# Optimization experiments

Hardware: AMD Instinct MI355X
Metric: run time of the kernel (lower is better)

## Reference

```python
import jax, jax.numpy as jnp
import numpy as np

B, S, E, D, H, L = 128, 50, 512, 1024, 16, 4
V, NU, NF, NR = 100000, 50000, 10000, 5
DK = D // H
FF = 4 * D


def _pe(S, D):
    # FranchisePositionalEncoding: two interleaved sin/cos halves (chrono + release*1.5)
    half = D // 2
    pos = jnp.arange(S, dtype=jnp.float32)[:, None]
    div = jnp.exp(jnp.arange(0, half, 2, dtype=jnp.float32) * (-np.log(10000.0) / half))
    def il(a):
        return jnp.stack([jnp.sin(a), jnp.cos(a)], axis=-1).reshape(S, half)
    return jnp.concatenate([il(pos * div), il(pos * div * 1.5)], axis=-1)  # [S, D]


def _ln(x, g, b):
    m = x.mean(-1, keepdims=True)
    v = ((x - m) ** 2).mean(-1, keepdims=True)
    return (x - m) * jax.lax.rsqrt(v + 1e-5) * g + b


def _gelu(x):
    return jax.nn.gelu(x, approximate=False)


def setup_inputs() -> dict:
    key = jax.random.key(0)
    ks = iter(jax.random.split(key, 64))
    def p(shape, s=0.02):
        return jax.random.normal(next(ks), shape, jnp.float32) * s
    inp = {
        'movie_table': p((V, E)), 'fran_table': p((NF, E)), 'entry_table': p((NR, E)),
        'proj_w': p((3 * E, D)), 'proj_b': jnp.zeros((D,), jnp.float32),
        'wq': p((L, D, D)), 'bq': jnp.zeros((L, D), jnp.float32),
        'wk': p((L, D, D)), 'bk': jnp.zeros((L, D), jnp.float32),
        'wv': p((L, D, D)), 'bv': jnp.zeros((L, D), jnp.float32),
        'wo': p((L, D, D)), 'bo': jnp.zeros((L, D), jnp.float32),
        'rel_table': p((L, NR, DK)),
        'aln_g': jnp.ones((L, D), jnp.float32), 'aln_b': jnp.zeros((L, D), jnp.float32),
        'f_w1': p((L, D, FF)), 'f_b1': jnp.zeros((L, FF), jnp.float32),
        'f_w2': p((L, FF, D)), 'f_b2': jnp.zeros((L, D), jnp.float32),
        'ln_g': jnp.ones((L, D), jnp.float32), 'ln_b': jnp.zeros((L, D), jnp.float32),
        'user_table': p((NU, D)),
        'mq_w': p((D, D)), 'mq_b': jnp.zeros((D,), jnp.float32),
        'mk_w': p((D, D)), 'mk_b': jnp.zeros((D,), jnp.float32),
        'mv_w': p((D, D)), 'mv_b': jnp.zeros((D,), jnp.float32),
        'mo_w': p((D, D)), 'mo_b': jnp.zeros((D,), jnp.float32),
        'c_w1': p((2 * D, D)), 'c_b1': jnp.zeros((D,), jnp.float32),
        'c_w2': p((D, 1)), 'c_b2': jnp.zeros((1,), jnp.float32),
        'n_w1': p((2 * D, D)), 'n_b1': jnp.zeros((D,), jnp.float32),
        'n_w2': p((D, V)), 'n_b2': jnp.zeros((V,), jnp.float32),
        'r_w1': p((3 * D, D)), 'r_b1': jnp.zeros((D,), jnp.float32),
        'r_w2': p((D, 1)), 'r_b2': jnp.zeros((1,), jnp.float32),
        'o_w1': p((D, D // 2)), 'o_b1': jnp.zeros((D // 2,), jnp.float32),
        'o_w2': p((D // 2, 2)), 'o_b2': jnp.zeros((2,), jnp.float32),
        'user_ids': jax.random.randint(next(ks), (B,), 0, NU),
        'movie_ids': jax.random.randint(next(ks), (B, S), 0, V),
        'franchise_ids': jax.random.randint(next(ks), (B, S), 0, NF),
        'entry_types': jax.random.randint(next(ks), (B, S), 0, NR),
        'relation_matrix': jax.random.randint(next(ks), (S, S), 0, NR),
    }
    return inp


def reference(movie_table, fran_table, entry_table, proj_w, proj_b,
              wq, bq, wk, bk, wv, bv, wo, bo, rel_table, aln_g, aln_b,
              f_w1, f_b1, f_w2, f_b2, ln_g, ln_b, user_table,
              mq_w, mq_b, mk_w, mk_b, mv_w, mv_b, mo_w, mo_b,
              c_w1, c_b1, c_w2, c_b2, n_w1, n_b1, n_w2, n_b2,
              r_w1, r_b1, r_w2, r_b2, o_w1, o_b1, o_w2, o_b2,
              user_ids, movie_ids, franchise_ids, entry_types, relation_matrix):
    b, s = movie_ids.shape
    d = proj_w.shape[1]
    nl, _, dk = rel_table.shape
    h = d // dk
    scale = 1.0 / np.sqrt(dk).astype(np.float32)

    # encoder input: concat(movie, franchise, entry) embeddings -> proj -> +PE
    x = jnp.concatenate([movie_table[movie_ids], fran_table[franchise_ids],
                         entry_table[entry_types]], axis=-1) @ proj_w + proj_b
    x = x + _pe(s, d)

    for l in range(nl):
        res = x
        q = (x @ wq[l] + bq[l]).reshape(b, s, h, dk).transpose(0, 2, 1, 3)  # [b,h,s,dk]
        k = (x @ wk[l] + bk[l]).reshape(b, s, h, dk).transpose(0, 2, 1, 3)
        v = (x @ wv[l] + bv[l]).reshape(b, s, h, dk).transpose(0, 2, 1, 3)
        scores = jnp.einsum('bhid,bhjd->bhij', q, k) * scale
        rel = rel_table[l][relation_matrix]  # [s,s,dk]
        scores = scores + 0.5 * jnp.einsum('bhid,ijd->bhij', q, rel)
        attn = jax.nn.softmax(scores, axis=-1)
        ctx = jnp.einsum('bhij,bhjd->bhid', attn, v).transpose(0, 2, 1, 3).reshape(b, s, d)
        x = _ln(ctx @ wo[l] + bo[l] + res, aln_g[l], aln_b[l])
        ff = _gelu(x @ f_w1[l] + f_b1[l]) @ f_w2[l] + f_b2[l]
        x = _ln(x + ff, ln_g[l], ln_b[l])

    # user preference cross-attention (nn.MultiheadAttention, q_len=1)
    user_emb = user_table[user_ids]  # [b,d]
    qh = (user_emb @ mq_w + mq_b).reshape(b, h, dk)
    kh = (x @ mk_w + mk_b).reshape(b, s, h, dk)
    vh = (x @ mv_w + mv_b).reshape(b, s, h, dk)
    a = jax.nn.softmax(jnp.einsum('bhd,bshd->bhs', qh, kh) * scale, axis=-1)
    user_pref = jnp.einsum('bhs,bshd->bhd', a, vh).reshape(b, d) @ mo_w + mo_b

    seq_repr = x.mean(axis=1)  # mask is None path
    ci = jnp.concatenate([user_pref, seq_repr], axis=-1)
    completion = jax.nn.sigmoid(_gelu(ci @ c_w1 + c_b1) @ c_w2 + c_b2)
    next_logits = _gelu(ci @ n_w1 + n_b1) @ n_w2 + n_b2
    ri = jnp.concatenate([user_emb, user_pref, seq_repr], axis=-1)
    rating = _gelu(ri @ r_w1 + r_b1) @ r_w2 + r_b2
    order = jax.nn.softmax(_gelu(user_pref @ o_w1 + o_b1) @ o_w2 + o_b2, axis=-1)
    return (x, completion, next_logits, rating, order, user_pref)
```

## Files before the change

kernel.cpp:

```cpp
#include <hip/hip_runtime.h>
#include <hip/hip_bf16.h>
#include <math.h>

#define B_   128
#define S_   50
#define BS_  (B_*S_)
#define E_   512
#define D_   1024
#define H_   16
#define DK_  64
#define L_   4
#define FF_  4096
#define V_   100000

typedef short bf8_t __attribute__((ext_vector_type(8)));
typedef float f32x4 __attribute__((ext_vector_type(4)));
typedef unsigned short u16;

__device__ __forceinline__ float gelu_exact(float x) {
    return 0.5f * x * (1.0f + erff(x * 0.70710678118654752440f));
}
__device__ __forceinline__ u16 f2bf(float f) {
    unsigned int u = __float_as_uint(f);
    return (u16)((u + 0x7FFFu + ((u >> 16) & 1u)) >> 16);
// ... 85 lines not shown
    const float* __restrict__ cb1, const float* __restrict__ nb1,
    const float* __restrict__ mkb, const float* __restrict__ mvb,
    float* __restrict__ bqkv, float* __restrict__ bcn, float* __restrict__ bkv,
    float* __restrict__ pet)
{
    int bi = blockIdx.x, tid = threadIdx.x;
    if (bi < 4) {
        for (int c = tid; c < 3072; c += 256) {
            float v = (c < 1024) ? bq[bi * 1024 + c]
                    : (c < 2048) ? bk[bi * 1024 + c - 1024]
                                 : bv[bi * 1024 + c - 2048];
            bqkv[bi * 3072 + c] = v;
        }
    } else if (bi == 4) {
        for (int c = tid; c < 2048; c += 256)
            bcn[c] = (c < 1024) ? cb1[c] : nb1[c - 1024];
    } else if (bi == 5) {
        for (int c = tid; c < 2048; c += 256)
            bkv[c] = (c < 1024) ? mkb[c] : mvb[c - 1024];
    } else {
        int s = bi - 6;
        const float cc = -logf(10000.0f) / 512.0f;
        for (int d = tid; d < D_; d += 256) {
            int second = d >= 512;
            int c2 = second ? d - 512 : d;
            int i = c2 >> 1;
            float div = expf(cc * (float)(2 * i));
            float aa = (float)s * div * (second ? 1.5f : 1.0f);
            pet[s * D_ + d] = (c2 & 1) ? cosf(aa) : sinf(aa);
        }
    }
}

template<int BM>
__global__ __launch_bounds__(256) void gemm_bf16_t(
    const u16* __restrict__ A, int lda, const u16* __restrict__ Wt,
    const float* __restrict__ bias, float* __restrict__ Cf,
    u16* __restrict__ Cb, int ldcb, u16* __restrict__ Cb2, int ldcb2,
    int N, int K, int act, const float* __restrict__ pe)
{
    constexpr int MR   = BM / 32;
    constexpr int AL   = BM / 64;
    constexpr int ABUF = BM * 32;
    __shared__ u16 As[2 * ABUF];
    __shared__ u16 Bs[2 * 4096];
    const int tid  = threadIdx.x;
    const int lane = tid & 63;
    const int wid  = tid >> 6;
    const int wr   = wid >> 1, wc = wid & 1;

    const int gx  = gridDim.x;
    const int nwg = gx * gridDim.y;
    int orig = blockIdx.y * gx + blockIdx.x;
    int qq = nwg >> 3, rr2 = nwg & 7, xcd = orig & 7, idx = orig >> 3;
    int wgid = (xcd < rr2) ? (xcd * (qq + 1) + idx)
                           : (rr2 * (qq + 1) + (xcd - rr2) * qq + idx);
    const int rowBase = (wgid / gx) * BM;
    const int colBase = (wgid % gx) * 128;

    const int fr = lane & 15;
    const int hi = lane >> 4;

    const int sRowL  = lane >> 2;
    const int sChunk = lane & 3;
    const int aRow0 = wid * (BM / 4) + sRowL;
    const int aKey  = (aRow0 >> 1) & 3;
    const u16* aS0 = A + (size_t)(rowBase + aRow0) * lda + ((sChunk ^ aKey) << 3);
    const u16* aS1 = aS0 + (size_t)16 * lda;
    const int ldsA0 = (wid * (BM / 4)) * 32;
    const int ldsA1 = ldsA0 + 512;
    const int bRow0 = wid * 32 + sRowL;
    const int bKey  = (bRow0 >> 1) & 3;
    const u16* bS0 = Wt + (size_t)(colBase + bRow0) * K + ((sChunk ^ bKey) << 3);
    const u16* bS1 = bS0 + (size_t)16 * K;
    const int ldsB0 = (wid * 32) * 32;
    const int ldsB1 = ldsB0 + 512;

    const int swz = ((hi ^ ((fr >> 1) & 3)) << 3);
    const int aRd = (wr * (BM / 2) + fr) * 32 + swz;
    const int bRd = (wc * 64 + fr) * 32 + swz;

    f32x4 acc[MR][4] = {};
    const int nk = K >> 5;

    auto STAGE = [&](int kb, int buf) {
        u16* dA = As + buf * ABUF;
        u16* dB = Bs + buf * 4096;
        gload16(aS0 + kb, dA + ldsA0);
        if constexpr (AL == 2) gload16(aS1 + kb, dA + ldsA1);
        gload16(bS0 + kb, dB + ldsB0);
        gload16(bS1 + kb, dB + ldsB1);
// ... 20 lines not shown
            bf[n] = *reinterpret_cast<const bf8_t*>(&bB[bRd + n * 512]);
        #pragma unroll
        for (int m = 0; m < MR; ++m)
            #pragma unroll
            for (int n = 0; n < 4; ++n)
                acc[m][n] = __builtin_amdgcn_mfma_f32_16x16x32_bf16(af[m], bf[n], acc[m][n], 0, 0, 0);
        if (t == nk - 1) break;
        __builtin_amdgcn_sched_barrier(0);
        asm volatile("s_waitcnt lgkmcnt(0)\n\ts_barrier" ::: "memory");
        __builtin_amdgcn_sched_barrier(0);
        if (t + 2 < nk) {
            STAGE((t + 2) << 5, cur);
            __builtin_amdgcn_sched_barrier(0);
            if constexpr (BM == 128) asm volatile("s_waitcnt vmcnt(4)\n\ts_barrier" ::: "memory");
            else                     asm volatile("s_waitcnt vmcnt(3)\n\ts_barrier" ::: "memory");
        } else {
            asm volatile("s_waitcnt vmcnt(0)\n\ts_barrier" ::: "memory");
        }
        __builtin_amdgcn_sched_barrier(0);
    }

    const int orow = hi << 2;
    #pragma unroll
    for (int m = 0; m < MR; ++m) {
        int r0 = rowBase + wr * (BM / 2) + m * 16 + orow;
        #pragma unroll
        for (int n = 0; n < 4; ++n) {
            int c = colBase + wc * 64 + n * 16 + fr;
            float bv = bias ? bias[c] : 0.0f;
            #pragma unroll
            for (int r = 0; r < 4; ++r) {
                float v = acc[m][n][r] + bv;
                if (act == 1) v = gelu_exact(v);
                if (pe) v += pe[(size_t)((r0 + r) % S_) * N + c];
                if (Cf)  Cf [(size_t)(r0 + r) * N + c] = v;
                if (Cb)  Cb [(size_t)(r0 + r) * ldcb  + c] = f2bf(v);
                if (Cb2) Cb2[(size_t)(r0 + r) * ldcb2 + c] = f2bf(v);
            }
        }
    }
}

__global__ __launch_bounds__(256) void gemm_logits(
    const float* __restrict__ A, int lda, const float* __restrict__ W,
    const float* __restrict__ bias, float* __restrict__ C, int N, int K)
{
    __shared__ u16 As[2][128][40];
    __shared__ u16 Bs[2][128][40];
    const int tid  = threadIdx.x;
    const int lane = tid & 63;
    const int wid  = tid >> 6;
    const int wr   = wid >> 1, wc = wid & 1;
    const int colBase = blockIdx.x * 128;

    const int a_r = tid >> 1;
    const int a_h = (tid & 1) << 4;
    const int b_c = tid & 127;
    const int b_h = (tid >> 7) << 4;

    const int fr = lane & 15;
    const int fk = (lane >> 4) << 3;

    f32x4 acc[4][4] = {};
    const int nvalid = N - colBase;
    const bool valid = b_c < nvalid;
    const int nk = K >> 5;

    float4 aR[4];
    float  bR[16];

    auto LD = [&](int kb) {
        const float* Ap = A + (size_t)a_r * lda + kb + a_h;
        #pragma unroll
        for (int q = 0; q < 4; ++q)
            aR[q] = *reinterpret_cast<const float4*>(Ap + q * 4);
        const float* Wp = W + (size_t)(kb + b_h) * N + colBase + b_c;
        #pragma unroll
        for (int kk = 0; kk < 16; ++kk)
            bR[kk] = valid ? Wp[(size_t)kk * N] : 0.0f;
    };
    auto ST = [&](int buf) {
        #pragma unroll
        for (int q = 0; q < 4; ++q) {
            ushort4 bb;
            bb.x = f2bf(aR[q].x); bb.y = f2bf(aR[q].y);
            bb.z = f2bf(aR[q].z); bb.w = f2bf(aR[q].w);
            *reinterpret_cast<ushort4*>(&As[buf][a_r][a_h + q * 4]) = bb;
        }
        u16 tmp[16];
        #pragma unroll
        for (int kk = 0; kk < 16; ++kk) tmp[kk] = f2bf(bR[kk]);
        *reinterpret_cast<bf8_t*>(&Bs[buf][b_c][b_h])     = *reinterpret_cast<const bf8_t*>(tmp);
        *reinterpret_cast<bf8_t*>(&Bs[buf][b_c][b_h + 8]) = *reinterpret_cast<const bf8_t*>(tmp + 8);
    };

    LD(0); ST(0);
    __syncthreads();

    for (int t = 0; t < nk; ++t) {
        if (t + 1 < nk) LD((t + 1) << 5);
        const int cur = t & 1;
        bf8_t af[4], bfv[4];
        #pragma unroll
        for (int m = 0; m < 4; ++m)
            af[m] = *reinterpret_cast<const bf8_t*>(&As[cur][wr * 64 + m * 16 + fr][fk]);
        #pragma unroll
        for (int n = 0; n < 4; ++n)
            bfv[n] = *reinterpret_cast<const bf8_t*>(&Bs[cur][wc * 64 + n * 16 + fr][fk]);
        #pragma unroll
        for (int m = 0; m < 4; ++m)
            #pragma unroll
            for (int n = 0; n < 4; ++n)
                acc[m][n] = __builtin_amdgcn_mfma_f32_16x16x32_bf16(af[m], bfv[n], acc[m][n], 0, 0, 0);
        if (t + 1 < nk) ST(cur ^ 1);
        __syncthreads();
    }

    const int orow = (lane >> 4) << 2;
    #pragma unroll
    for (int m = 0; m < 4; ++m) {
        int r0 = wr * 64 + m * 16 + orow;
        #pragma unroll
        for (int n = 0; n < 4; ++n) {
            int c = colBase + wc * 64 + n * 16 + fr;
            if (c < N) {
                float bv = bias ? bias[c] : 0.0f;
                #pragma unroll
                for (int r = 0; r < 4; ++r)
                    C[(size_t)(r0 + r) * N + c] = acc[m][n][r] + bv;
            }
        }
    }
}

__global__ __launch_bounds__(256) void attn_kernel(
    const u16* __restrict__ qkv, const float* __restrict__ rt, const int* __restrict__ rm,
    u16* __restrict__ ctxb)
{
    int bh = blockIdx.x;
    int b = bh >> 4, h = bh & 15;
    __shared__ float qs[S_][DK_ + 1], ks[S_][DK_ + 1], vs[S_][DK_ + 1];
    __shared__ float rts[5][DK_];
    __shared__ float Rs[S_][8];
    int tid = threadIdx.x;
    int wave = tid >> 6, lane = tid & 63;

    for (int idx = tid; idx < S_ * DK_; idx += 256) {
        int s = idx >> 6, d = idx & 63;
        size_t g = ((size_t)(b * S_ + s)) * (3 * D_) + h * DK_ + d;
        qs[s][d] = bf2f(qkv[g]);
        ks[s][d] = bf2f(qkv[g + D_]);
        vs[s][d] = bf2f(qkv[g + 2 * D_]);
    }
    for (int i = tid; i < 5 * DK_; i += 256)
        rts[i >> 6][i & 63] = rt[i];
    __syncthreads();

    for (int t = tid; t < S_ * 5; t += 256) {
        int i = t / 5, r = t - 5 * i;
        float a = 0.0f;
        #pragma unroll 8
        for (int d = 0; d < DK_; ++d) a += qs[i][d] * rts[r][d];
        Rs[i][r] = a;
    }
    __syncthreads();

    const float scale = 0.125f;
    for (int i = wave; i < S_; i += 4) {
        float sc = -INFINITY;
        if (lane < S_) {
            float acc = 0.0f;
            #pragma unroll 8
            for (int d = 0; d < DK_; ++d) acc += qs[i][d] * ks[lane][d];
            sc = acc * scale + 0.5f * Rs[i][rm[i * S_ + lane]];
        }
        float m = sc;
        #pragma unroll
        for (int off = 32; off; off >>= 1) m = fmaxf(m, __shfl_xor(m, off));
        float e = (lane < S_) ? expf(sc - m) : 0.0f;
        float sum = e;
        #pragma unroll
        for (int off = 32; off; off >>= 1) sum += __shfl_xor(sum, off);
        float aval = e / sum;

        float acc = 0.0f;
        for (int j = 0; j < S_; ++j) {
            float aj = __shfl(aval, j);
            acc += aj * vs[j][lane];
        }
        ctxb[((size_t)(b * S_ + i)) * D_ + h * DK_ + lane] = f2bf(acc);
    }
}

__global__ __launch_bounds__(256) void add_ln(
    const u16* __restrict__ a, const u16* __restrict__ res,
    const float* __restrict__ g, const float* __restrict__ be,
    u16* __restrict__ outb, float* __restrict__ outf)
{
    int row = blockIdx.x, tid = threadIdx.x;
    int c0 = tid << 2;
    ushort4 va = *reinterpret_cast<const ushort4*>(a   + (size_t)row * D_ + c0);
    ushort4 vr = *reinterpret_cast<const ushort4*>(res + (size_t)row * D_ + c0);
    float vals[4] = { bf2f(va.x) + bf2f(vr.x), bf2f(va.y) + bf2f(vr.y),
                      bf2f(va.z) + bf2f(vr.z), bf2f(va.w) + bf2f(vr.w) };
    float s = vals[0] + vals[1] + vals[2] + vals[3];
    __shared__ float red[8];
    #pragma unroll
    for (int off = 32; off; off >>= 1) s += __shfl_xor(s, off);
    int wave = tid >> 6, lane = tid & 63;
    if (lane == 0) red[wave] = s;
    __syncthreads();
    float mean = (red[0] + red[1] + red[2] + red[3]) * (1.0f / D_);
    float vv = 0.0f;
    #pragma unroll
    for (int t = 0; t < 4; ++t) {
        float d = vals[t] - mean;
        vv += d * d;
    }
    #pragma unroll
    for (int off = 32; off; off >>= 1) vv += __shfl_xor(vv, off);
    if (lane == 0) red[4 + wave] = vv;
    __syncthreads();
    float var = (red[4] + red[5] + red[6] + red[7]) * (1.0f / D_);
    float rstd = rsqrtf(var + 1e-5f);
    float4 gv  = *reinterpret_cast<const float4*>(g  + c0);
    float4 bev = *reinterpret_cast<const float4*>(be + c0);
    float o0 = (vals[0] - mean) * rstd * gv.x + bev.x;
    float o1 = (vals[1] - mean) * rstd * gv.y + bev.y;
    float o2 = (vals[2] - mean) * rstd * gv.z + bev.z;
    float o3 = (vals[3] - mean) * rstd * gv.w + bev.w;
    ushort4 ob;
    ob.x = f2bf(o0); ob.y = f2bf(o1); ob.z = f2bf(o2); ob.w = f2bf(o3);
    *reinterpret_cast<ushort4*>(outb + (size_t)row * D_ + c0) = ob;
    if (outf) {
        float4 of = { o0, o1, o2, o3 };
        *reinterpret_cast<float4*>(outf + (size_t)row * D_ + c0) = of;
    }
}

__global__ __launch_bounds__(256) void gather_user(
    const float* __restrict__ ut, const int* __restrict__ ids,
    u16* __restrict__ o1, int ld1, u16* __restrict__ o2, int ld2)
{
    int b = blockIdx.x;
    int uid = ids[b];
    for (int d = threadIdx.x; d < D_; d += 256) {
        u16 v = f2bf(ut[(size_t)uid * D_ + d]);
        o1[(size_t)b * ld1 + d] = v;
        o2[(size_t)b * ld2 + d] = v;
    }
}

__global__ __launch_bounds__(64) void cross_attn(
    const u16* __restrict__ qh, const u16* __restrict__ kv, u16* __restrict__ up)
{
    int bh = blockIdx.x;
    int b = bh >> 4, h = bh & 15;
    int lane = threadIdx.x;
    __shared__ float qv[DK_];
    qv[lane] = bf2f(qh[(size_t)b * D_ + h * DK_ + lane]);
    __syncthreads();
    float sc = -INFINITY;
    if (lane < S_) {
        float acc = 0.0f;
        const u16* krow = kv + ((size_t)(b * S_ + lane)) * 2048 + h * DK_;
        #pragma unroll 8
        for (int d = 0; d < DK_; ++d) acc += qv[d] * bf2f(krow[d]);
        sc = acc * 0.125f;
    }
// ... 115 lines not shown
    const float* r_b1        = (const float*)d_in[40];
    const float* r_w2        = (const float*)d_in[41];
    const float* r_b2        = (const float*)d_in[42];
    const float* o_w1        = (const float*)d_in[43];
    const float* o_b1        = (const float*)d_in[44];
    const float* o_w2        = (const float*)d_in[45];
    const float* o_b2        = (const float*)d_in[46];
    const int* user_ids      = (const int*)d_in[47];
    const int* movie_ids     = (const int*)d_in[48];
    const int* franchise_ids = (const int*)d_in[49];
    const int* entry_types   = (const int*)d_in[50];
    const int* relation_mat  = (const int*)d_in[51];

    u16* up16 = (u16*)d_ws;
    u16* proj_wt = up16;
    u16* wqkv_t  = proj_wt + (size_t)1024 * 1536;
    u16* wo_t    = wqkv_t  + (size_t)4 * 3072 * 1024;
    u16* fw1_buf = wo_t    + (size_t)4 * 1024 * 1024;
    u16* fw2_buf = fw1_buf + (size_t)4096 * 1024;
    u16* mq_t    = fw2_buf + (size_t)1024 * 4096;
    u16* mk_t    = mq_t    + (size_t)1024 * 1024;
    u16* mv_t    = mk_t    + (size_t)1024 * 1024;
    u16* mo_t    = mv_t    + (size_t)1024 * 1024;
    u16* cn_w1t  = mo_t    + (size_t)1024 * 1024;
    u16* r_w1t   = cn_w1t  + (size_t)2048 * 2048;
    u16* o_w1t   = r_w1t   + (size_t)1024 * 3072;
    u16* ffb     = o_w1t   + (size_t)512 * 1024;
    u16* xinb    = ffb;
    u16* xb      = ffb     + (size_t)BS_ * FF_;
    u16* xb2     = xb      + (size_t)BS_ * D_;
    u16* qkvb    = xb2     + (size_t)BS_ * D_;
    u16* kvb     = qkvb    + (size_t)BS_ * 3 * D_;
    u16* ctxb    = kvb;
    u16* ob      = kvb     + (size_t)BS_ * D_;
    u16* ueb     = kvb     + (size_t)BS_ * 2 * D_;
    u16* upb_pre = ueb     + (size_t)B_ * D_;
    u16* cib     = upb_pre + (size_t)B_ * D_;
    u16* rib     = cib     + (size_t)B_ * 2 * D_;
    float* fp    = (float*)(rib + (size_t)B_ * 3 * D_);
    float* bqkv  = fp;
    float* bcn   = bqkv + 4 * 3072;
    float* bkv   = bcn  + 2048;
    float* pet   = bkv  + 2048;
    float* h1cn  = pet  + 50 * 1024;
    float* h1r   = h1cn + (size_t)B_ * 2048;
    float* ho    = h1r  + (size_t)B_ * D_;

    float* xout    = (float*)d_out;
    float* comp    = xout + (size_t)BS_ * D_;
    float* logits  = comp + B_;
    float* rating  = logits + (size_t)B_ * V_;
    float* order   = rating + B_;
    float* upref   = order + 2 * B_;

    dim3 blk(256);

    wtrans<<<dim3(32, 48, 1), blk, 0, stream>>>(proj_w, proj_wt, 1536, 1024, 0, 0, 0);
    wtrans_qkv<<<dim3(32, 32, 12), blk, 0, stream>>>(wq, wk, wv, wqkv_t);
    WT8 w8;
    w8.s[0] = wo;                 w8.d[0] = wo_t;
    w8.s[1] = wo + 1048576;       w8.d[1] = wo_t + 1048576;
    w8.s[2] = wo + 2097152;       w8.d[2] = wo_t + 2097152;
    w8.s[3] = wo + 3145728;       w8.d[3] = wo_t + 3145728;
    w8.s[4] = mq_w;               w8.d[4] = mq_t;
    w8.s[5] = mk_w;               w8.d[5] = mk_t;
    w8.s[6] = mv_w;               w8.d[6] = mv_t;
    w8.s[7] = mo_w;               w8.d[7] = mo_t;
    wtrans8<<<dim3(32, 32, 8), blk, 0, stream>>>(w8);
    wtrans<<<dim3(32, 64, 1), blk, 0, stream>>>(c_w1, cn_w1t, 2048, 1024, 0, 0, 0);
    wtrans<<<dim3(32, 64, 1), blk, 0, stream>>>(n_w1, cn_w1t, 2048, 1024, 0, 0, 1024);
    wtrans<<<dim3(32, 96, 1), blk, 0, stream>>>(r_w1, r_w1t, 3072, 1024, 0, 0, 0);
    wtrans<<<dim3(16, 32, 1), blk, 0, stream>>>(o_w1, o_w1t, 1024, 512, 0, 0, 0);
    setup_misc<<<dim3(56), blk, 0, stream>>>(bq, bk, bv, c_b1, n_b1, mk_b, mv_b,
                                             bqkv, bcn, bkv, pet);

    embed_concat<<<BS_, blk, 0, stream>>>(movie_table, fran_table, entry_table,
                                          movie_ids, franchise_ids, entry_types, xinb);
    gemm_bf16_t<64><<<dim3(8, 100), blk, 0, stream>>>(xinb, 1536, proj_wt, proj_b,
                                                      nullptr, xb, 1024, nullptr, 0,
                                                      D_, 1536, 0, pet);

    for (int l = 0; l < L_; ++l) {
        gemm_bf16_t<128><<<dim3(24, 50), blk, 0, stream>>>(xb, 1024,
                wqkv_t + (size_t)l * 3145728, bqkv + l * 3072,
                nullptr, qkvb, 3072, nullptr, 0, 3 * D_, D_, 0, nullptr);
        attn_kernel<<<B_ * H_, blk, 0, stream>>>(qkvb, rel_table + (size_t)l * 5 * DK_,
                                                 relation_mat, ctxb);
        gemm_bf16_t<64><<<dim3(8, 100), blk, 0, stream>>>(ctxb, 1024,
                wo_t + (size_t)l * 1048576, bo + l * D_,
                nullptr, ob, 1024, nullptr, 0, D_, D_, 0, nullptr);
        add_ln<<<BS_, blk, 0, stream>>>(ob, xb, aln_g + l * D_, aln_b + l * D_, xb2, nullptr);
        wtrans_ff<<<dim3(128, 32, 2), blk, 0, stream>>>(f_w1 + (size_t)l * D_ * FF_,
                                                        f_w2 + (size_t)l * FF_ * D_,
                                                        fw1_buf, fw2_buf);
        gemm_bf16_t<128><<<dim3(32, 50), blk, 0, stream>>>(xb2, 1024, fw1_buf, f_b1 + l * FF_,
                nullptr, ffb, 4096, nullptr, 0, FF_, D_, 1, nullptr);
        gemm_bf16_t<64><<<dim3(8, 100), blk, 0, stream>>>(ffb, 4096, fw2_buf, f_b2 + l * D_,
                nullptr, ob, 1024, nullptr, 0, D_, FF_, 0, nullptr);
        add_ln<<<BS_, blk, 0, stream>>>(ob, xb2, ln_g + l * D_, ln_b + l * D_, xb,
                                        (l == L_ - 1) ? xout : nullptr);
    }

    gather_user<<<B_, blk, 0, stream>>>(user_table, user_ids, ueb, 1024, rib, 3072);
    gemm_bf16_t<64><<<dim3(8, 2), blk, 0, stream>>>(ueb, 1024, mq_t, mq_b,
            nullptr, qkvb, 1024, nullptr, 0, D_, D_, 0, nullptr);
    gemm_bf16_t<64><<<dim3(16, 100), blk, 0, stream>>>(xb, 1024, mk_t, bkv,
            nullptr, kvb, 2048, nullptr, 0, 2 * D_, D_, 0, nullptr);
    cross_attn<<<B_ * H_, dim3(64), 0, stream>>>(qkvb, kvb, upb_pre);
    gemm_bf16_t<64><<<dim3(8, 2), blk, 0, stream>>>(upb_pre, 1024, mo_t, mo_b,
            upref, cib, 2048, rib + 1024, 3072, D_, D_, 0, nullptr);

    seq_mean<<<B_, blk, 0, stream>>>(xout, cib + 1024, 2048, rib + 2048, 3072);

    gemm_bf16_t<64><<<dim3(16, 2), blk, 0, stream>>>(cib, 2048, cn_w1t, bcn,
            h1cn, nullptr, 0, nullptr, 0, 2048, 2048, 1, nullptr);
    gemm_bf16_t<64><<<dim3(8, 2), blk, 0, stream>>>(rib, 3072, r_w1t, r_b1,
            h1r, nullptr, 0, nullptr, 0, D_, 3072, 1, nullptr);
    gemm_bf16_t<64><<<dim3(4, 2), blk, 0, stream>>>(cib, 2048, o_w1t, o_b1,
            ho, nullptr, 0, nullptr, 0, 512, D_, 1, nullptr);
    gemm_logits<<<dim3(782, 1), blk, 0, stream>>>(h1cn + 1024, 2048, n_w2, n_b2,
                                                  logits, V_, D_);
    heads_final<<<B_, blk, 0, stream>>>(h1cn, h1r, ho, c_w2, c_b2, r_w2, r_b2,
                                        o_w2, o_b2, comp, rating, order);
}
```

Measured before the change: 2.283 ms.

## Split-K 128x128 GEMM for N=1024 projections with fused bias/residual LayerNorm combine

Replaces the 64-row-tile GEMMs with N=1024 outputs (input projection, Wo, FF2) by a 128x128 split-K kernel. The kernel splits K in two across blockIdx.z, writes fp32 partials, and reorders workgroups to be XCD-aware. The partials are summed with bias (plus positional encoding or residual add and LayerNorm) in new combine kernels. The cross-attention KV GEMM also moves to 128-row tiles. This aims to raise per-block data reuse while keeping enough blocks in flight, at the cost of extra fp32 partial traffic that reuses scratch buffers.

```diff
diff --git a/kernel.cpp b/kernel.cpp
--- a/kernel.cpp
+++ b/kernel.cpp
@@ -261,168 +261,148 @@
     }
 }
 
-__global__ __launch_bounds__(256) void gemm_logits(
-    const float* __restrict__ A, int lda, const float* __restrict__ W,
-    const float* __restrict__ bias, float* __restrict__ C, int N, int K)
-{
-    __shared__ u16 As[2][128][40];
-    __shared__ u16 Bs[2][128][40];
+__global__ __launch_bounds__(256) void gemm_sk(
+    const u16* __restrict__ A, int lda, const u16* __restrict__ Wt, int ldb,
+    float* __restrict__ P0, float* __restrict__ P1,
+    int N, int Kh)
+{
+    __shared__ u16 As[2 * 4096];
+    __shared__ u16 Bs[2 * 4096];
     const int tid  = threadIdx.x;
     const int lane = tid & 63;
     const int wid  = tid >> 6;
     const int wr   = wid >> 1, wc = wid & 1;
-    const int colBase = blockIdx.x * 128;
-
-    const int a_r = tid >> 1;
-    const int a_h = (tid & 1) << 4;
-    const int b_c = tid & 127;
-    const int b_h = (tid >> 7) << 4;
+
+    const int gx  = gridDim.x;
+    const int nwg = gx * gridDim.y;
+    int orig = blockIdx.y * gx + blockIdx.x;
+    int qq = nwg >> 3, rr2 = nwg & 7, xcd = orig & 7, idx = orig >> 3;
+    int wgid = (xcd < rr2) ? (xcd * (qq + 1) + idx)
+                           : (rr2 * (qq + 1) + (xcd - rr2) * qq + idx);
+    const int rowBase = (wgid / gx) * 128;
+    const int colBase = (wgid % gx) * 128;
+    const int k0 = blockIdx.z * Kh;
+    float* P = blockIdx.z ? P1 : P0;
 
     const int fr = lane & 15;
-    const int fk = (lane >> 4) << 3;
+    const int hi = lane >> 4;
+
+    const int sRowL  = lane >> 2;
+    const int sChunk = lane & 3;
+    const int gRow0  = (wid << 5) + sRowL;
+    const int skey   = (gRow0 >> 1) & 3;
+    const int gC     = (sChunk ^ skey) << 3;
+    const u16* aS0 = A  + (size_t)(rowBase + gRow0) * lda + k0 + gC;
+    const u16* aS1 = aS0 + (size_t)16 * lda;
+    const u16* bS0 = Wt + (size_t)(colBase + gRow0) * ldb + k0 + gC;
+    const u16* bS1 = bS0 + (size_t)16 * ldb;
+    const int ldsW0 = (wid << 5) << 5;
+    const int ldsW1 = ldsW0 + (16 << 5);
+
+    const int swz = ((hi ^ ((fr >> 1) & 3)) << 3);
+    const int aRd = (wr * 64 + fr) * 32 + swz;
+    const int bRd = (wc * 64 + fr) * 32 + swz;
 
     f32x4 acc[4][4] = {};
-    const int nvalid = N - colBase;
-    const bool valid = b_c < nvalid;
-    const int nk = K >> 5;
-
-    float4 aR[4];
-    float  bR[16];
-
-    auto LD = [&](int kb) {
-        const float* Ap = A + (size_t)a_r * lda + kb + a_h;
-        #pragma unroll
-        for (int q = 0; q < 4; ++q)
-            aR[q] = *reinterpret_cast<const float4*>(Ap + q * 4);
-        const float* Wp = W + (size_t)(kb + b_h) * N + colBase + b_c;
-        #pragma unroll
-        for (int kk = 0; kk < 16; ++kk)
-            bR[kk] = valid ? Wp[(size_t)kk * N] : 0.0f;
+    const int nk = Kh >> 5;
+
+    auto STAGE = [&](int kb, int buf) {
+        u16* dA = As + buf * 4096;
+        u16* dB = Bs + buf * 4096;
+        gload16(aS0 + kb, dA + ldsW0);
+        gload16(aS1 + kb, dA + ldsW1);
+        gload16(bS0 + kb, dB + ldsW0);
+        gload16(bS1 + kb, dB + ldsW1);
     };
-    auto ST = [&](int buf) {
-        #pragma unroll
-        for (int q = 0; q < 4; ++q) {
-            ushort4 bb;
-            bb.x = f2bf(aR[q].x); bb.y = f2bf(aR[q].y);
-            bb.z = f2bf(aR[q].z); bb.w = f2bf(aR[q].w);
-            *reinterpret_cast<ushort4*>(&As[buf][a_r][a_h + q * 4]) = bb;
-        }
-        u16 tmp[16];
-        #pragma unroll
-        for (int kk = 0; kk < 16; ++kk) tmp[kk] = f2bf(bR[kk]);
-        *reinterpret_cast<bf8_t*>(&Bs[buf][b_c][b_h])     = *reinterpret_cast<const bf8_t*>(tmp);
-        *reinterpret_cast<bf8_t*>(&Bs[buf][b_c][b_h + 8]) = *reinterpret_cast<const bf8_t*>(tmp + 8);
-    };
-
-    LD(0); ST(0);
-    __syncthreads();
+
+    STAGE(0, 0);
+    __builtin_amdgcn_sched_barrier(0);
+    STAGE(32, 1);
+    __builtin_amdgcn_sched_barrier(0);
+    asm volatile("s_waitcnt vmcnt(4)\n\ts_barrier" ::: "memory");
+    __builtin_amdgcn_sched_barrier(0);
 
     for (int t = 0; t < nk; ++t) {
-        if (t + 1 < nk) LD((t + 1) << 5);
         const int cur = t & 1;
-        bf8_t af[4], bfv[4];
+        const u16* bA = As + cur * 4096;
+        const u16* bB = Bs + cur * 4096;
+        bf8_t af[4], bf[4];
         #pragma unroll
         for (int m = 0; m < 4; ++m)
-            af[m] = *reinterpret_cast<const bf8_t*>(&As[cur][wr * 64 + m * 16 + fr][fk]);
+            af[m] = *reinterpret_cast<const bf8_t*>(&bA[aRd + m * 512]);
         #pragma unroll
         for (int n = 0; n < 4; ++n)
-            bfv[n] = *reinterpret_cast<const bf8_t*>(&Bs[cur][wc * 64 + n * 16 + fr][fk]);
+            bf[n] = *reinterpret_cast<const bf8_t*>(&bB[bRd + n * 512]);
         #pragma unroll
         for (int m = 0; m < 4; ++m)
             #pragma unroll
             for (int n = 0; n < 4; ++n)
-                acc[m][n] = __builtin_amdgcn_mfma_f32_16x16x32_bf16(af[m], bfv[n], acc[m][n], 0, 0, 0);
-        if (t + 1 < nk) ST(cur ^ 1);
-        __syncthreads();
-    }
-
-    const int orow = (lane >> 4) << 2;
+                acc[m][n] = __builtin_amdgcn_mfma_f32_16x16x32_bf16(af[m], bf[n], acc[m][n], 0, 0, 0);
+        if (t == nk - 1) break;
+        __builtin_amdgcn_sched_barrier(0);
+        asm volatile("s_waitcnt lgkmcnt(0)\n\ts_barrier" ::: "memory");
+        __builtin_amdgcn_sched_barrier(0);
+        if (t + 2 < nk) {
+            STAGE((t + 2) << 5, cur);
+            __builtin_amdgcn_sched_barrier(0);
+            asm volatile("s_waitcnt vmcnt(4)\n\ts_barrier" ::: "memory");
+        } else {
+            asm volatile("s_waitcnt vmcnt(0)\n\ts_barrier" ::: "memory");
+        }
+        __builtin_amdgcn_sched_barrier(0);
+    }
+
+    const int orow = hi << 2;
     #pragma unroll
     for (int m = 0; m < 4; ++m) {
-        int r0 = wr * 64 + m * 16 + orow;
+        int r0 = rowBase + wr * 64 + m * 16 + orow;
         #pragma unroll
         for (int n = 0; n < 4; ++n) {
             int c = colBase + wc * 64 + n * 16 + fr;
-            if (c < N) {
-                float bv = bias ? bias[c] : 0.0f;
-                #pragma unroll
-                for (int r = 0; r < 4; ++r)
-                    C[(size_t)(r0 + r) * N + c] = acc[m][n][r] + bv;
-            }
-        }
-    }
-}
-
-__global__ __launch_bounds__(256) void attn_kernel(
-    const u16* __restrict__ qkv, const float* __restrict__ rt, const int* __restrict__ rm,
-    u16* __restrict__ ctxb)
-{
-    int bh = blockIdx.x;
-    int b = bh >> 4, h = bh & 15;
-    __shared__ float qs[S_][DK_ + 1], ks[S_][DK_ + 1], vs[S_][DK_ + 1];
-    __shared__ float rts[5][DK_];
-    __shared__ float Rs[S_][8];
-    int tid = threadIdx.x;
-    int wave = tid >> 6, lane = tid & 63;
-
-    for (int idx = tid; idx < S_ * DK_; idx += 256) {
-        int s = idx >> 6, d = idx & 63;
-        size_t g = ((size_t)(b * S_ + s)) * (3 * D_) + h * DK_ + d;
-        qs[s][d] = bf2f(qkv[g]);
-        ks[s][d] = bf2f(qkv[g + D_]);
-        vs[s][d] = bf2f(qkv[g + 2 * D_]);
-    }
-    for (int i = tid; i < 5 * DK_; i += 256)
-        rts[i >> 6][i & 63] = rt[i];
-    __syncthreads();
-
-    for (int t = tid; t < S_ * 5; t += 256) {
-        int i = t / 5, r = t - 5 * i;
-        float a = 0.0f;
-        #pragma unroll 8
-        for (int d = 0; d < DK_; ++d) a += qs[i][d] * rts[r][d];
-        Rs[i][r] = a;
-    }
-    __syncthreads();
-
-    const float scale = 0.125f;
-    for (int i = wave; i < S_; i += 4) {
-        float sc = -INFINITY;
-        if (lane < S_) {
-            float acc = 0.0f;
-            #pragma unroll 8
-            for (int d = 0; d < DK_; ++d) acc += qs[i][d] * ks[lane][d];
-            sc = acc * scale + 0.5f * Rs[i][rm[i * S_ + lane]];
-        }
-        float m = sc;
-        #pragma unroll
-        for (int off = 32; off; off >>= 1) m = fmaxf(m, __shfl_xor(m, off));
-        float e = (lane < S_) ? expf(sc - m) : 0.0f;
-        float sum = e;
-        #pragma unroll
-        for (int off = 32; off; off >>= 1) sum += __shfl_xor(sum, off);
-        float aval = e / sum;
-
-        float acc = 0.0f;
-        for (int j = 0; j < S_; ++j) {
-            float aj = __shfl(aval, j);
-            acc += aj * vs[j][lane];
-        }
-        ctxb[((size_t)(b * S_ + i)) * D_ + h * DK_ + lane] = f2bf(acc);
-    }
-}
-
-__global__ __launch_bounds__(256) void add_ln(
-    const u16* __restrict__ a, const u16* __restrict__ res,
+            #pragma unroll
+            for (int r = 0; r < 4; ++r)
+                P[(size_t)(r0 + r) * N + c] = acc[m][n][r];
+        }
+    }
+}
+
+__global__ __launch_bounds__(256) void combine_bias_pe(
+    const float* __restrict__ p1, const float* __restrict__ p2,
+    const float* __restrict__ bias, const float* __restrict__ pe,
+    u16* __restrict__ outb)
+{
+    int row = blockIdx.x, tid = threadIdx.x;
+    int c0 = tid << 2;
+    size_t base = (size_t)row * D_ + c0;
+    float4 v1 = *reinterpret_cast<const float4*>(p1 + base);
+    float4 v2 = *reinterpret_cast<const float4*>(p2 + base);
+    float4 bv = *reinterpret_cast<const float4*>(bias + c0);
+    float4 pv = *reinterpret_cast<const float4*>(pe + (size_t)(row % S_) * D_ + c0);
+    ushort4 ob;
+    ob.x = f2bf(v1.x + v2.x + bv.x + pv.x);
+    ob.y = f2bf(v1.y + v2.y + bv.y + pv.y);
+    ob.z = f2bf(v1.z + v2.z + bv.z + pv.z);
+    ob.w = f2bf(v1.w + v2.w + bv.w + pv.w);
+    *reinterpret_cast<ushort4*>(outb + base) = ob;
+}
+
+__global__ __launch_bounds__(256) void add_ln2(
+    const float* __restrict__ p1, const float* __restrict__ p2,
+    const float* __restrict__ bias, const u16* __restrict__ res,
     const float* __restrict__ g, const float* __restrict__ be,
     u16* __restrict__ outb, float* __restrict__ outf)
 {
     int row = blockIdx.x, tid = threadIdx.x;
     int c0 = tid << 2;
-    ushort4 va = *reinterpret_cast<const ushort4*>(a   + (size_t)row * D_ + c0);
-    ushort4 vr = *reinterpret_cast<const ushort4*>(res + (size_t)row * D_ + c0);
-    float vals[4] = { bf2f(va.x) + bf2f(vr.x), bf2f(va.y) + bf2f(vr.y),
-                      bf2f(va.z) + bf2f(vr.z), bf2f(va.w) + bf2f(vr.w) };
+    size_t base = (size_t)row * D_ + c0;
+    float4 v1 = *reinterpret_cast<const float4*>(p1 + base);
+    float4 v2 = *reinterpret_cast<const float4*>(p2 + base);
+    float4 bv = *reinterpret_cast<const float4*>(bias + c0);
+    ushort4 vr = *reinterpret_cast<const ushort4*>(res + base);
+    float vals[4] = { v1.x + v2.x + bv.x + bf2f(vr.x),
+                      v1.y + v2.y + bv.y + bf2f(vr.y),
+                      v1.z + v2.z + bv.z + bf2f(vr.z),
+                      v1.w + v2.w + bv.w + bf2f(vr.w) };
     float s = vals[0] + vals[1] + vals[2] + vals[3];
     __shared__ float red[8];
     #pragma unroll
@@ -451,10 +431,161 @@
     float o3 = (vals[3] - mean) * rstd * gv.w + bev.w;
     ushort4 ob;
     ob.x = f2bf(o0); ob.y = f2bf(o1); ob.z = f2bf(o2); ob.w = f2bf(o3);
-    *reinterpret_cast<ushort4*>(outb + (size_t)row * D_ + c0) = ob;
+    *reinterpret_cast<ushort4*>(outb + base) = ob;
     if (outf) {
         float4 of = { o0, o1, o2, o3 };
-        *reinterpret_cast<float4*>(outf + (size_t)row * D_ + c0) = of;
+        *reinterpret_cast<float4*>(outf + base) = of;
+    }
+}
+
+__global__ __launch_bounds__(256) void gemm_logits(
+    const float* __restrict__ A, int lda, const float* __restrict__ W,
+    const float* __restrict__ bias, float* __restrict__ C, int N, int K)
+{
+    __shared__ u16 As[2][128][40];
+    __shared__ u16 Bs[2][128][40];
+    const int tid  = threadIdx.x;
+    const int lane = tid & 63;
+    const int wid  = tid >> 6;
+    const int wr   = wid >> 1, wc = wid & 1;
+    const int colBase = blockIdx.x * 128;
+
+    const int a_r = tid >> 1;
+    const int a_h = (tid & 1) << 4;
+    const int b_c = tid & 127;
+    const int b_h = (tid >> 7) << 4;
+
+    const int fr = lane & 15;
+    const int fk = (lane >> 4) << 3;
+
+    f32x4 acc[4][4] = {};
+    const int nvalid = N - colBase;
+    const bool valid = b_c < nvalid;
+    const int nk = K >> 5;
+
+    float4 aR[4];
+    float  bR[16];
+
+    auto LD = [&](int kb) {
+        const float* Ap = A + (size_t)a_r * lda + kb + a_h;
+        #pragma unroll
+        for (int q = 0; q < 4; ++q)
+            aR[q] = *reinterpret_cast<const float4*>(Ap + q * 4);
+        const float* Wp = W + (size_t)(kb + b_h) * N + colBase + b_c;
+        #pragma unroll
+        for (int kk = 0; kk < 16; ++kk)
+            bR[kk] = valid ? Wp[(size_t)kk * N] : 0.0f;
+    };
+    auto ST = [&](int buf) {
+        #pragma unroll
+        for (int q = 0; q < 4; ++q) {
+            ushort4 bb;
+            bb.x = f2bf(aR[q].x); bb.y = f2bf(aR[q].y);
+            bb.z = f2bf(aR[q].z); bb.w = f2bf(aR[q].w);
+            *reinterpret_cast<ushort4*>(&As[buf][a_r][a_h + q * 4]) = bb;
+        }
+        u16 tmp[16];
+        #pragma unroll
+        for (int kk = 0; kk < 16; ++kk) tmp[kk] = f2bf(bR[kk]);
+        *reinterpret_cast<bf8_t*>(&Bs[buf][b_c][b_h])     = *reinterpret_cast<const bf8_t*>(tmp);
+        *reinterpret_cast<bf8_t*>(&Bs[buf][b_c][b_h + 8]) = *reinterpret_cast<const bf8_t*>(tmp + 8);
+    };
+
+    LD(0); ST(0);
+    __syncthreads();
+
+    for (int t = 0; t < nk; ++t) {
+        if (t + 1 < nk) LD((t + 1) << 5);
+        const int cur = t & 1;
+        bf8_t af[4], bfv[4];
+        #pragma unroll
+        for (int m = 0; m < 4; ++m)
+            af[m] = *reinterpret_cast<const bf8_t*>(&As[cur][wr * 64 + m * 16 + fr][fk]);
+        #pragma unroll
+        for (int n = 0; n < 4; ++n)
+            bfv[n] = *reinterpret_cast<const bf8_t*>(&Bs[cur][wc * 64 + n * 16 + fr][fk]);
+        #pragma unroll
+        for (int m = 0; m < 4; ++m)
+            #pragma unroll
+            for (int n = 0; n < 4; ++n)
+                acc[m][n] = __builtin_amdgcn_mfma_f32_16x16x32_bf16(af[m], bfv[n], acc[m][n], 0, 0, 0);
+        if (t + 1 < nk) ST(cur ^ 1);
+        __syncthreads();
+    }
+
+    const int orow = (lane >> 4) << 2;
+    #pragma unroll
+    for (int m = 0; m < 4; ++m) {
+        int r0 = wr * 64 + m * 16 + orow;
+        #pragma unroll
+        for (int n = 0; n < 4; ++n) {
+            int c = colBase + wc * 64 + n * 16 + fr;
+            if (c < N) {
+                float bv = bias ? bias[c] : 0.0f;
+                #pragma unroll
+                for (int r = 0; r < 4; ++r)
+                    C[(size_t)(r0 + r) * N + c] = acc[m][n][r] + bv;
+            }
+        }
+    }
+}
+
+__global__ __launch_bounds__(256) void attn_kernel(
+    const u16* __restrict__ qkv, const float* __restrict__ rt, const int* __restrict__ rm,
+    u16* __restrict__ ctxb)
+{
+    int bh = blockIdx.x;
+    int b = bh >> 4, h = bh & 15;
+    __shared__ float qs[S_][DK_ + 1], ks[S_][DK_ + 1], vs[S_][DK_ + 1];
+    __shared__ float rts[5][DK_];
+    __shared__ float Rs[S_][8];
+    int tid = threadIdx.x;
+    int wave = tid >> 6, lane = tid & 63;
+
+    for (int idx = tid; idx < S_ * DK_; idx += 256) {
+        int s = idx >> 6, d = idx & 63;
+        size_t g = ((size_t)(b * S_ + s)) * (3 * D_) + h * DK_ + d;
+        qs[s][d] = bf2f(qkv[g]);
+        ks[s][d] = bf2f(qkv[g + D_]);
+        vs[s][d] = bf2f(qkv[g + 2 * D_]);
+    }
+    for (int i = tid; i < 5 * DK_; i += 256)
+        rts[i >> 6][i & 63] = rt[i];
+    __syncthreads();
+
+    for (int t = tid; t < S_ * 5; t += 256) {
+        int i = t / 5, r = t - 5 * i;
+        float a = 0.0f;
+        #pragma unroll 8
+        for (int d = 0; d < DK_; ++d) a += qs[i][d] * rts[r][d];
+        Rs[i][r] = a;
+    }
+    __syncthreads();
+
+    const float scale = 0.125f;
+    for (int i = wave; i < S_; i += 4) {
+        float sc = -INFINITY;
+        if (lane < S_) {
+            float acc = 0.0f;
+            #pragma unroll 8
+            for (int d = 0; d < DK_; ++d) acc += qs[i][d] * ks[lane][d];
+            sc = acc * scale + 0.5f * Rs[i][rm[i * S_ + lane]];
+        }
+        float m = sc;
+        #pragma unroll
+        for (int off = 32; off; off >>= 1) m = fmaxf(m, __shfl_xor(m, off));
+        float e = (lane < S_) ? expf(sc - m) : 0.0f;
+        float sum = e;
+        #pragma unroll
+        for (int off = 32; off; off >>= 1) sum += __shfl_xor(sum, off);
+        float aval = e / sum;
+
+        float acc = 0.0f;
+        for (int j = 0; j < S_; ++j) {
+            float aj = __shfl(aval, j);
+            acc += aj * vs[j][lane];
+        }
+        ctxb[((size_t)(b * S_ + i)) * D_ + h * DK_ + lane] = f2bf(acc);
     }
 }
 
@@ -636,7 +767,6 @@
     u16* qkvb    = xb2     + (size_t)BS_ * D_;
     u16* kvb     = qkvb    + (size_t)BS_ * 3 * D_;
     u16* ctxb    = kvb;
-    u16* ob      = kvb     + (size_t)BS_ * D_;
     u16* ueb     = kvb     + (size_t)BS_ * 2 * D_;
     u16* upb_pre = ueb     + (size_t)B_ * D_;
     u16* cib     = upb_pre + (size_t)B_ * D_;
@@ -649,6 +779,10 @@
     float* h1cn  = pet  + 50 * 1024;
     float* h1r   = h1cn + (size_t)B_ * 2048;
     float* ho    = h1r  + (size_t)B_ * D_;
+
+    float* pQK = (float*)qkvb;
+    float* pKV = (float*)kvb;
+    float* pFF = (float*)ffb;
 
     float* xout    = (float*)d_out;
     float* comp    = xout + (size_t)BS_ * D_;
@@ -680,9 +814,9 @@
 
     embed_concat<<<BS_, blk, 0, stream>>>(movie_table, fran_table, entry_table,
                                           movie_ids, franchise_ids, entry_types, xinb);
-    gemm_bf16_t<64><<<dim3(8, 100), blk, 0, stream>>>(xinb, 1536, proj_wt, proj_b,
-                                                      nullptr, xb, 1024, nullptr, 0,
-                                                      D_, 1536, 0, pet);
+    gemm_sk<<<dim3(8, 50, 2), blk, 0, stream>>>(xinb, 1536, proj_wt, 1536,
+                                                pQK, pKV, D_, 768);
+    combine_bias_pe<<<BS_, blk, 0, stream>>>(pQK, pKV, proj_b, pet, xb);
 
     for (int l = 0; l < L_; ++l) {
         gemm_bf16_t<128><<<dim3(24, 50), blk, 0, stream>>>(xb, 1024,
@@ -690,25 +824,26 @@
                 nullptr, qkvb, 3072, nullptr, 0, 3 * D_, D_, 0, nullptr);
         attn_kernel<<<B_ * H_, blk, 0, stream>>>(qkvb, rel_table + (size_t)l * 5 * DK_,
                                                  relation_mat, ctxb);
-        gemm_bf16_t<64><<<dim3(8, 100), blk, 0, stream>>>(ctxb, 1024,
-                wo_t + (size_t)l * 1048576, bo + l * D_,
-                nullptr, ob, 1024, nullptr, 0, D_, D_, 0, nullptr);
-        add_ln<<<BS_, blk, 0, stream>>>(ob, xb, aln_g + l * D_, aln_b + l * D_, xb2, nullptr);
+        gemm_sk<<<dim3(8, 50, 2), blk, 0, stream>>>(ctxb, 1024,
+                wo_t + (size_t)l * 1048576, 1024, pQK, pFF, D_, 512);
+        add_ln2<<<BS_, blk, 0, stream>>>(pQK, pFF, bo + l * D_, xb,
+                                         aln_g + l * D_, aln_b + l * D_, xb2, nullptr);
         wtrans_ff<<<dim3(128, 32, 2), blk, 0, stream>>>(f_w1 + (size_t)l * D_ * FF_,
                                                         f_w2 + (size_t)l * FF_ * D_,
                                                         fw1_buf, fw2_buf);
         gemm_bf16_t<128><<<dim3(32, 50), blk, 0, stream>>>(xb2, 1024, fw1_buf, f_b1 + l * FF_,
                 nullptr, ffb, 4096, nullptr, 0, FF_, D_, 1, nullptr);
-        gemm_bf16_t<64><<<dim3(8, 100), blk, 0, stream>>>(ffb, 4096, fw2_buf, f_b2 + l * D_,
-                nullptr, ob, 1024, nullptr, 0, D_, FF_, 0, nullptr);
-        add_ln<<<BS_, blk, 0, stream>>>(ob, xb2, ln_g + l * D_, ln_b + l * D_, xb,
-                                        (l == L_ - 1) ? xout : nullptr);
+        gemm_sk<<<dim3(8, 50, 2), blk, 0, stream>>>(ffb, 4096, fw2_buf, 4096,
+                                                    pQK, pKV, D_, 2048);
+        add_ln2<<<BS_, blk, 0, stream>>>(pQK, pKV, f_b2 + l * D_, xb2,
+                                         ln_g + l * D_, ln_b + l * D_, xb,
+                                         (l == L_ - 1) ? xout : nullptr);
     }
 
     gather_user<<<B_, blk, 0, stream>>>(user_table, user_ids, ueb, 1024, rib, 3072);
     gemm_bf16_t<64><<<dim3(8, 2), blk, 0, stream>>>(ueb, 1024, mq_t, mq_b,
             nullptr, qkvb, 1024, nullptr, 0, D_, D_, 0, nullptr);
-    gemm_bf16_t<64><<<dim3(16, 100), blk, 0, stream>>>(xb, 1024, mk_t, bkv,
+    gemm_bf16_t<128><<<dim3(16, 50), blk, 0, stream>>>(xb, 1024, mk_t, bkv,
             nullptr, kvb, 2048, nullptr, 0, 2 * D_, D_, 0, nullptr);
     cross_attn<<<B_ * H_, dim3(64), 0, stream>>>(qkvb, kvb, upb_pre);
     gemm_bf16_t<64><<<dim3(8, 2), blk, 0, stream>>>(upb_pre, 1024, mo_t, mo_b,
```

Result: faster. 2.192 ms (-4.0%).

## Add 256x256-tile 512-thread GEMM kernel for large transformer matmuls

Applied to the files above, without the earlier changes.

Adds a new bf16 MFMA GEMM kernel with 256x256 output tiles, 8 waves, a BK of 64 and double-buffered LDS with XOR swizzle. It replaces the 64/128-row tile GEMM for the input projection, QKV, output projection, both FFN matmuls and the cross-attention K/V projection. Larger tiles raise arithmetic intensity and data reuse per workgroup, but produce far fewer workgroups (e.g. 100 for N=1024), which may underfill the 256 CUs. They also use 128KB of LDS and a large accumulator array, which limits occupancy. The old kernel loses its XCD remap and its PE epilogue, which were only needed for the large calls.

```diff
diff --git a/kernel.cpp b/kernel.cpp
--- a/kernel.cpp
+++ b/kernel.cpp
@@ -141,12 +141,122 @@
     }
 }
 
+__global__ __launch_bounds__(512, 2) void gemm256(
+    const u16* __restrict__ A, int lda, const u16* __restrict__ Wt,
+    const float* __restrict__ bias,
+    u16* __restrict__ Cb, int ldcb,
+    int N, int K, int act, const float* __restrict__ pe)
+{
+    __shared__ u16 As[2 * 16384];
+    __shared__ u16 Bs[2 * 16384];
+    const int tid  = threadIdx.x;
+    const int lane = tid & 63;
+    const int wid  = tid >> 6;
+    const int wr   = wid >> 2;
+    const int wc   = wid & 3;
+
+    const int gx  = gridDim.x;
+    const int nwg = gx * gridDim.y;
+    int orig = blockIdx.y * gx + blockIdx.x;
+    int qq = nwg >> 3, rr2 = nwg & 7, xcd = orig & 7, idx = orig >> 3;
+    int wgid = (xcd < rr2) ? (xcd * (qq + 1) + idx)
+                           : (rr2 * (qq + 1) + (xcd - rr2) * qq + idx);
+    const int rowBase = (wgid / gx) * 256;
+    const int colBase = (wgid % gx) * 256;
+
+    const int fr = lane & 15;
+    const int hi = lane >> 4;
+
+    const int sRow  = lane >> 3;
+    const int sChk  = (lane & 7) ^ sRow;
+    const u16* aB = A  + (size_t)(rowBase + wid * 32 + sRow) * lda + sChk * 8;
+    const u16* bB = Wt + (size_t)(colBase + wid * 32 + sRow) * K   + sChk * 8;
+    const size_t aRowStep = (size_t)8 * lda;
+    const size_t bRowStep = (size_t)8 * K;
+
+    const int pa0 = hi ^ (fr & 7);
+    const int aRd0 = (wr * 128 + fr) * 64 + pa0 * 8;
+    const int aRd1 = (wr * 128 + fr) * 64 + (pa0 ^ 4) * 8;
+    const int pb0 = hi ^ (fr & 7);
+    const int bRd0 = (wc * 64 + fr) * 64 + pb0 * 8;
+    const int bRd1 = (wc * 64 + fr) * 64 + (pb0 ^ 4) * 8;
+
+    f32x4 acc[8][4] = {};
+    const int nk = K >> 6;
+
+    u16* Acur = As;          u16* Bcur = Bs;
+    u16* Anxt = As + 16384;  u16* Bnxt = Bs + 16384;
+
+    auto STAGE = [&](int kb, u16* dA, u16* dB) {
+        #pragma unroll
+        for (int i = 0; i < 4; ++i)
+            gload16(aB + kb + i * aRowStep, dA + (wid * 32 + i * 8) * 64);
+        #pragma unroll
+        for (int i = 0; i < 4; ++i)
+            gload16(bB + kb + i * bRowStep, dB + (wid * 32 + i * 8) * 64);
+    };
+
+    STAGE(0, Acur, Bcur);
+    __builtin_amdgcn_sched_barrier(0);
+    asm volatile("s_waitcnt vmcnt(0)\n\ts_barrier" ::: "memory");
+    __builtin_amdgcn_sched_barrier(0);
+
+    for (int t = 0; t < nk; ++t) {
+        if (t + 1 < nk) {
+            STAGE((t + 1) << 6, Anxt, Bnxt);
+            __builtin_amdgcn_sched_barrier(0);
+        }
+        bf8_t bf0[4], bf1[4];
+        #pragma unroll
+        for (int n = 0; n < 4; ++n) {
+            bf0[n] = *reinterpret_cast<const bf8_t*>(&Bcur[bRd0 + n * 1024]);
+            bf1[n] = *reinterpret_cast<const bf8_t*>(&Bcur[bRd1 + n * 1024]);
+        }
+        __builtin_amdgcn_s_setprio(1);
+        #pragma unroll
+        for (int m = 0; m < 8; ++m) {
+            bf8_t a0 = *reinterpret_cast<const bf8_t*>(&Acur[aRd0 + m * 1024]);
+            bf8_t a1 = *reinterpret_cast<const bf8_t*>(&Acur[aRd1 + m * 1024]);
+            #pragma unroll
+            for (int n = 0; n < 4; ++n) {
+                acc[m][n] = __builtin_amdgcn_mfma_f32_16x16x32_bf16(a0, bf0[n], acc[m][n], 0, 0, 0);
+                acc[m][n] = __builtin_amdgcn_mfma_f32_16x16x32_bf16(a1, bf1[n], acc[m][n], 0, 0, 0);
+            }
+        }
+        __builtin_amdgcn_s_setprio(0);
+        if (t == nk - 1) break;
+        __builtin_amdgcn_sched_barrier(0);
+        asm volatile("s_waitcnt vmcnt(0) lgkmcnt(0)\n\ts_barrier" ::: "memory");
+        __builtin_amdgcn_sched_barrier(0);
+        u16* tp;
+        tp = Acur; Acur = Anxt; Anxt = tp;
+        tp = Bcur; Bcur = Bnxt; Bnxt = tp;
+    }
+
+    #pragma unroll
+    for (int m = 0; m < 8; ++m) {
+        int r0 = rowBase + wr * 128 + m * 16 + hi * 4;
+        #pragma unroll
+        for (int n = 0; n < 4; ++n) {
+            int c = colBase + wc * 64 + n * 16 + fr;
+            float bv = bias ? bias[c] : 0.0f;
+            #pragma unroll
+            for (int r = 0; r < 4; ++r) {
+                float v = acc[m][n][r] + bv;
+                if (act == 1) v = gelu_exact(v);
+                if (pe) v += pe[(size_t)((r0 + r) % S_) * 1024 + c];
+                Cb[(size_t)(r0 + r) * ldcb + c] = f2bf(v);
+            }
+        }
+    }
+}
+
 template<int BM>
 __global__ __launch_bounds__(256) void gemm_bf16_t(
     const u16* __restrict__ A, int lda, const u16* __restrict__ Wt,
     const float* __restrict__ bias, float* __restrict__ Cf,
     u16* __restrict__ Cb, int ldcb, u16* __restrict__ Cb2, int ldcb2,
-    int N, int K, int act, const float* __restrict__ pe)
+    int N, int K, int act)
 {
     constexpr int MR   = BM / 32;
     constexpr int AL   = BM / 64;
@@ -158,14 +268,8 @@
     const int wid  = tid >> 6;
     const int wr   = wid >> 1, wc = wid & 1;
 
-    const int gx  = gridDim.x;
-    const int nwg = gx * gridDim.y;
-    int orig = blockIdx.y * gx + blockIdx.x;
-    int qq = nwg >> 3, rr2 = nwg & 7, xcd = orig & 7, idx = orig >> 3;
-    int wgid = (xcd < rr2) ? (xcd * (qq + 1) + idx)
-                           : (rr2 * (qq + 1) + (xcd - rr2) * qq + idx);
-    const int rowBase = (wgid / gx) * BM;
-    const int colBase = (wgid % gx) * 128;
+    const int rowBase = blockIdx.y * BM;
+    const int colBase = blockIdx.x * 128;
 
     const int fr = lane & 15;
     const int hi = lane >> 4;
@@ -252,7 +356,6 @@
             for (int r = 0; r < 4; ++r) {
                 float v = acc[m][n][r] + bv;
                 if (act == 1) v = gelu_exact(v);
-                if (pe) v += pe[(size_t)((r0 + r) % S_) * N + c];
                 if (Cf)  Cf [(size_t)(r0 + r) * N + c] = v;
                 if (Cb)  Cb [(size_t)(r0 + r) * ldcb  + c] = f2bf(v);
                 if (Cb2) Cb2[(size_t)(r0 + r) * ldcb2 + c] = f2bf(v);
@@ -658,6 +761,7 @@
     float* upref   = order + 2 * B_;
 
     dim3 blk(256);
+    dim3 blk512(512);
 
     wtrans<<<dim3(32, 48, 1), blk, 0, stream>>>(proj_w, proj_wt, 1536, 1024, 0, 0, 0);
     wtrans_qkv<<<dim3(32, 32, 12), blk, 0, stream>>>(wq, wk, wv, wqkv_t);
@@ -680,48 +784,47 @@
 
     embed_concat<<<BS_, blk, 0, stream>>>(movie_table, fran_table, entry_table,
                                           movie_ids, franchise_ids, entry_types, xinb);
-    gemm_bf16_t<64><<<dim3(8, 100), blk, 0, stream>>>(xinb, 1536, proj_wt, proj_b,
-                                                      nullptr, xb, 1024, nullptr, 0,
-                                                      D_, 1536, 0, pet);
+    gemm256<<<dim3(4, 25), blk512, 0, stream>>>(xinb, 1536, proj_wt, proj_b,
+                                                xb, 1024, D_, 1536, 0, pet);
 
     for (int l = 0; l < L_; ++l) {
-        gemm_bf16_t<128><<<dim3(24, 50), blk, 0, stream>>>(xb, 1024,
+        gemm256<<<dim3(12, 25), blk512, 0, stream>>>(xb, 1024,
                 wqkv_t + (size_t)l * 3145728, bqkv + l * 3072,
-                nullptr, qkvb, 3072, nullptr, 0, 3 * D_, D_, 0, nullptr);
+                qkvb, 3072, 3 * D_, D_, 0, nullptr);
         attn_kernel<<<B_ * H_, blk, 0, stream>>>(qkvb, rel_table + (size_t)l * 5 * DK_,
                                                  relation_mat, ctxb);
-        gemm_bf16_t<64><<<dim3(8, 100), blk, 0, stream>>>(ctxb, 1024,
+        gemm256<<<dim3(4, 25), blk512, 0, stream>>>(ctxb, 1024,
                 wo_t + (size_t)l * 1048576, bo + l * D_,
-                nullptr, ob, 1024, nullptr, 0, D_, D_, 0, nullptr);
+                ob, 1024, D_, D_, 0, nullptr);
         add_ln<<<BS_, blk, 0, stream>>>(ob, xb, aln_g + l * D_, aln_b + l * D_, xb2, nullptr);
         wtrans_ff<<<dim3(128, 32, 2), blk, 0, stream>>>(f_w1 + (size_t)l * D_ * FF_,
                                                         f_w2 + (size_t)l * FF_ * D_,
                                                         fw1_buf, fw2_buf);
-        gemm_bf16_t<128><<<dim3(32, 50), blk, 0, stream>>>(xb2, 1024, fw1_buf, f_b1 + l * FF_,
-                nullptr, ffb, 4096, nullptr, 0, FF_, D_, 1, nullptr);
-        gemm_bf16_t<64><<<dim3(8, 100), blk, 0, stream>>>(ffb, 4096, fw2_buf, f_b2 + l * D_,
-                nullptr, ob, 1024, nullptr, 0, D_, FF_, 0, nullptr);
+        gemm256<<<dim3(16, 25), blk512, 0, stream>>>(xb2, 1024, fw1_buf, f_b1 + l * FF_,
+                ffb, 4096, FF_, D_, 1, nullptr);
+        gemm256<<<dim3(4, 25), blk512, 0, stream>>>(ffb, 4096, fw2_buf, f_b2 + l * D_,
+                ob, 1024, D_, FF_, 0, nullptr);
         add_ln<<<BS_, blk, 0, stream>>>(ob, xb2, ln_g + l * D_, ln_b + l * D_, xb,
                                         (l == L_ - 1) ? xout : nullptr);
     }
 
     gather_user<<<B_, blk, 0, stream>>>(user_table, user_ids, ueb, 1024, rib, 3072);
     gemm_bf16_t<64><<<dim3(8, 2), blk, 0, stream>>>(ueb, 1024, mq_t, mq_b,
-            nullptr, qkvb, 1024, nullptr, 0, D_, D_, 0, nullptr);
-    gemm_bf16_t<64><<<dim3(16, 100), blk, 0, stream>>>(xb, 1024, mk_t, bkv,
-            nullptr, kvb, 2048, nullptr, 0, 2 * D_, D_, 0, nullptr);
+            nullptr, qkvb, 1024, nullptr, 0, D_, D_, 0);
+    gemm256<<<dim3(8, 25), blk512, 0, stream>>>(xb, 1024, mk_t, bkv,
+            kvb, 2048, 2 * D_, D_, 0, nullptr);
     cross_attn<<<B_ * H_, dim3(64), 0, stream>>>(qkvb, kvb, upb_pre);
     gemm_bf16_t<64><<<dim3(8, 2), blk, 0, stream>>>(upb_pre, 1024, mo_t, mo_b,
-            upref, cib, 2048, rib + 1024, 3072, D_, D_, 0, nullptr);
+            upref, cib, 2048, rib + 1024, 3072, D_, D_, 0);
 
     seq_mean<<<B_, blk, 0, stream>>>(xout, cib + 1024, 2048, rib + 2048, 3072);
 
     gemm_bf16_t<64><<<dim3(16, 2), blk, 0, stream>>>(cib, 2048, cn_w1t, bcn,
-            h1cn, nullptr, 0, nullptr, 0, 2048, 2048, 1, nullptr);
+            h1cn, nullptr, 0, nullptr, 0, 2048, 2048, 1);
     gemm_bf16_t<64><<<dim3(8, 2), blk, 0, stream>>>(rib, 3072, r_w1t, r_b1,
-            h1r, nullptr, 0, nullptr, 0, D_, 3072, 1, nullptr);
+            h1r, nullptr, 0, nullptr, 0, D_, 3072, 1);
     gemm_bf16_t<64><<<dim3(4, 2), blk, 0, stream>>>(cib, 2048, o_w1t, o_b1,
-            ho, nullptr, 0, nullptr, 0, 512, D_, 1, nullptr);
+            ho, nullptr, 0, nullptr, 0, 512, D_, 1);
     gemm_logits<<<dim3(782, 1), blk, 0, stream>>>(h1cn + 1024, 2048, n_w2, n_b2,
                                                   logits, V_, D_);
     heads_final<<<B_, blk, 0, stream>>>(h1cn, h1r, ho, c_w2, c_b2, r_w2, r_b2,
```

Measured after the change: 2.345 ms. +2.7%, slower.
